# Performance work log

Measured on AMD Instinct MI355X. Metric: run time of the kernel, lower is better.

## Reference

```python
import jax, jax.numpy as jnp
import numpy as np

B, N, D = 32, 32768, 128

def setup_inputs() -> dict:
    key = jax.random.key(0)
    k1, k2, k3 = jax.random.split(key, 3)
    inputs = jax.random.normal(k1, (B, D), dtype=jnp.float32)
    # alphas must be in (0,1): variance = 1 - alpha
    alphas = jax.random.uniform(k2, (B,), dtype=jnp.float32, minval=0.05, maxval=0.95)
    data_batch = jax.random.normal(k3, (N, D), dtype=jnp.float32)
    return {"inputs": inputs, "alphas": alphas, "data_batch": data_batch}

def reference(inputs, alphas, data_batch):
    # inputs: [B, D], alphas: [B], data_batch: [N, D]
    d = inputs.shape[-1]
    sqrt_a = jnp.sqrt(alphas)[:, None]          # [B, 1]
    var = (1.0 - alphas)[:, None]                # [B, 1]
    # means = sqrt(alpha) * data -> [B, N, D]; squared distance summed over D
    diff = inputs[:, None, :] - sqrt_a[:, :, None] * data_batch[None]  # [B, N, D]
    sq = jnp.sum(diff * diff, axis=-1)           # [B, N]
    # logits summed over feature dim: -(0.5*D*log(var) + 0.5/var * sq)
    logits = -(0.5 * d * jnp.log(var) + 0.5 / var * sq)  # [B, N]
    probs = jax.nn.softmax(logits, axis=1)       # [B, N]
    x0 = probs @ data_batch                      # [B, D]
    return (inputs - sqrt_a * x0) / jnp.sqrt(var)
```

## Files before the change

### kernel.cpp

```cpp
#include <hip/hip_runtime.h>
#include <math.h>

#define BB 32
#define DD 128
#define NN 32768

#define NB 1024
#define RPB 32
#define NP NB
#define WS_MS_OFF ((size_t)BB * NB * DD)

typedef __attribute__((ext_vector_type(8))) short bf16x8;
typedef __attribute__((ext_vector_type(4))) float f32x4;

#define O_RH   0
#define O_RL   8192
#define O_INH  16384
#define O_INL  24576
#define O_RT   32768
#define O_NRM  40960
#define O_LQ   41088
#define ARENA  45184
#define O_PT   O_INH
#define O_X0   O_RH

__device__ __forceinline__ unsigned bf16_rne(float x) {
    unsigned u = __builtin_bit_cast(unsigned, x);
    return (u + 0x7FFFu + ((u >> 16) & 1u)) >> 16;
}
__device__ __forceinline__ float bf16f(unsigned h) {
    return __builtin_bit_cast(float, h << 16);
}
__device__ __forceinline__ unsigned pk2(float a, float b) {
    return bf16_rne(a) | (bf16_rne(b) << 16);
}

__global__ __launch_bounds__(256) void bayes_k1(
    const float* __restrict__ inputs, const float* __restrict__ alphas,
    const float* __restrict__ data, float* __restrict__ ws)
{
    __shared__ __align__(16) char arena[ARENA];

    const int tid  = threadIdx.x;
    const int lane = tid & 63;
    const int wv   = tid >> 6;
    const int ln   = lane & 15;
    const int g    = lane >> 4;
    const int bid  = blockIdx.x;

    {
        const int r = tid >> 3, c8 = tid & 7;
        const float4* gp = (const float4*)(data + ((size_t)bid * RPB + r) * DD + c8 * 16);
        float v[16];
        #pragma unroll
        for (int i = 0; i < 4; ++i) {
            const float4 t4 = gp[i];
            v[4*i+0] = t4.x; v[4*i+1] = t4.y; v[4*i+2] = t4.z; v[4*i+3] = t4.w;
        }
        float nn = 0.0f;
        #pragma unroll
        for (int i = 0; i < 16; ++i) nn = fmaf(v[i], v[i], nn);
        nn += __shfl_xor(nn, 1);
        nn += __shfl_xor(nn, 2);
        nn += __shfl_xor(nn, 4);
        if (c8 == 0) *(float*)(arena + O_NRM + r * 4) = nn;

        const int swz = (r & 7) << 4;
        #pragma unroll
        for (int u = 0; u < 2; ++u) {
            unsigned hw[4], lw[4];
            #pragma unroll
            for (int j = 0; j < 4; ++j) {
                const float a = v[u*8 + 2*j], b = v[u*8 + 2*j + 1];
                const unsigned ah = bf16_rne(a), bh = bf16_rne(b);
                hw[j] = ah | (bh << 16);
                lw[j] = pk2(a - bf16f(ah), b - bf16f(bh));
            }
            const int go = (c8 * 32 + u * 16) ^ swz;
            *(uint4*)(arena + O_RH + r * 256 + go) = make_uint4(hw[0], hw[1], hw[2], hw[3]);
            *(uint4*)(arena + O_RL + r * 256 + go) = make_uint4(lw[0], lw[1], lw[2], lw[3]);
        }
    }

    {
        const int b = tid >> 3, c8 = tid & 7;
        const float4* gp = (const float4*)(inputs + b * DD + c8 * 16);
        float v[16];
        #pragma unroll
        for (int i = 0; i < 4; ++i) {
            const float4 t4 = gp[i];
            v[4*i+0] = t4.x; v[4*i+1] = t4.y; v[4*i+2] = t4.z; v[4*i+3] = t4.w;
        }
        const int swz = (b & 7) << 4;
        #pragma unroll
        for (int u = 0; u < 2; ++u) {
            unsigned hw[4], lw[4];
            #pragma unroll
            for (int j = 0; j < 4; ++j) {
                const float a = v[u*8 + 2*j], bb = v[u*8 + 2*j + 1];
                const unsigned ah = bf16_rne(a), bh = bf16_rne(bb);
                hw[j] = ah | (bh << 16);
                lw[j] = pk2(a - bf16f(ah), bb - bf16f(bh));
            }
            const int go = (c8 * 32 + u * 16) ^ swz;
            *(uint4*)(arena + O_INH + b * 256 + go) = make_uint4(hw[0], hw[1], hw[2], hw[3]);
            *(uint4*)(arena + O_INL + b * 256 + go) = make_uint4(lw[0], lw[1], lw[2], lw[3]);
        }
    }

    {
        const int d = tid >> 1, rh = tid & 1;
        const float* gc = data + ((size_t)bid * RPB + rh * 16) * DD + d;
        const int swz = (d & 3) << 4;
        #pragma unroll
        for (int u = 0; u < 2; ++u) {
            unsigned w[4];
            #pragma unroll
            for (int j = 0; j < 4; ++j)
                w[j] = pk2(gc[(u*8 + 2*j) * DD], gc[(u*8 + 2*j + 1) * DD]);
            *(uint4*)(arena + O_RT + d * 64 + ((rh * 32 + u * 16) ^ swz)) =
                make_uint4(w[0], w[1], w[2], w[3]);
        }
    }
    __syncthreads();

    {
        const int mt = wv >> 1, nt = wv & 1;
        const int r  = mt * 16 + ln;
        const int b2 = nt * 16 + ln;
        f32x4 acc1;
        #pragma unroll
        for (int i = 0; i < 4; ++i) acc1[i] = 0.0f;

        #pragma unroll
        for (int ks = 0; ks < 4; ++ks) {
            const int kbyte = ks * 64 + g * 16;
            const bf16x8 Bh = *(const bf16x8*)(arena + O_INH + b2 * 256 + (kbyte ^ ((b2 & 7) << 4)));
            const bf16x8 Bl = *(const bf16x8*)(arena + O_INL + b2 * 256 + (kbyte ^ ((b2 & 7) << 4)));
            const bf16x8 Ah = *(const bf16x8*)(arena + O_RH  + r  * 256 + (kbyte ^ ((r  & 7) << 4)));
            const bf16x8 Al = *(const bf16x8*)(arena + O_RL  + r  * 256 + (kbyte ^ ((r  & 7) << 4)));
            acc1 = __builtin_amdgcn_mfma_f32_16x16x32_bf16(Ah, Bh, acc1, 0, 0, 0);
            acc1 = __builtin_amdgcn_mfma_f32_16x16x32_bf16(Al, Bh, acc1, 0, 0, 0);
            acc1 = __builtin_amdgcn_mfma_f32_16x16x32_bf16(Ah, Bl, acc1, 0, 0, 0);
        }
        #pragma unroll
        for (int i = 0; i < 4; ++i)
            *(float*)(arena + O_LQ + (((mt * 16 + g * 4 + i) * 32) + nt * 16 + ln) * 4) = acc1[i];
    }
    __syncthreads();

    if (wv < 2) {
        const int b = wv * 16 + ln;
        const float alpha = alphas[b];
        const float var = 1.0f - alpha;
        const float c1 = sqrtf(alpha) / var;
        const float c2 = 0.5f * alpha / var;

        float lg[8];
        float mx = -1e30f;
        #pragma unroll
        for (int j = 0; j < 8; ++j) {
            const int r = g * 8 + j;
            const float L  = *(const float*)(arena + O_LQ + (r * 32 + b) * 4);
            const float nr = *(const float*)(arena + O_NRM + r * 4);
            lg[j] = fmaf(c1, L, -c2 * nr);
            mx = fmaxf(mx, lg[j]);
        }
        mx = fmaxf(mx, __shfl_xor(mx, 16));
        mx = fmaxf(mx, __shfl_xor(mx, 32));

        float e[8];
        float ss = 0.0f;
        #pragma unroll
        for (int j = 0; j < 8; ++j) { e[j] = __expf(lg[j] - mx); ss += e[j]; }
        ss += __shfl_xor(ss, 16);
        ss += __shfl_xor(ss, 32);

        *(uint4*)(arena + O_PT + b * 64 + ((g * 16) ^ ((b & 3) << 4))) =
            make_uint4(pk2(e[0], e[1]), pk2(e[2], e[3]), pk2(e[4], e[5]), pk2(e[6], e[7]));
        if (g == 0)
            *(float2*)(ws + WS_MS_OFF + ((size_t)b * NB + bid) * 2) = make_float2(mx, ss);
    }
    __syncthreads();

    {
        f32x4 acc2[2][2];
        #pragma unroll
        for (int a = 0; a < 2; ++a)
            #pragma unroll
            for (int c = 0; c < 2; ++c)
                #pragma unroll
                for (int i = 0; i < 4; ++i) acc2[a][c][i] = 0.0f;

        bf16x8 Bp[2];
        #pragma unroll
        for (int nt = 0; nt < 2; ++nt) {
            const int b2 = nt * 16 + ln;
            Bp[nt] = *(const bf16x8*)(arena + O_PT + b2 * 64 + ((g * 16) ^ ((b2 & 3) << 4)));
        }
        #pragma unroll
        for (int a = 0; a < 2; ++a) {
            const int d = (wv * 2 + a) * 16 + ln;
            const bf16x8 Ar = *(const bf16x8*)(arena + O_RT + d * 64 + ((g * 16) ^ ((d & 3) << 4)));
            #pragma unroll
            for (int nt = 0; nt < 2; ++nt)
                acc2[a][nt] = __builtin_amdgcn_mfma_f32_16x16x32_bf16(Ar, Bp[nt], acc2[a][nt], 0, 0, 0);
        }
        #pragma unroll
        for (int a = 0; a < 2; ++a)
            #pragma unroll
            for (int nt = 0; nt < 2; ++nt) {
                const int b  = nt * 16 + ln;
                const int d0 = (wv * 2 + a) * 16 + g * 4;
                *(f32x4*)(arena + O_X0 + b * 512 + ((d0 * 4) ^ ((b & 7) << 4))) = acc2[a][nt];
            }
    }
    __syncthreads();

    {
        const int b = tid >> 3, c8 = tid & 7;
        const int swz = (b & 7) << 4;
        float* dst = ws + ((size_t)b * NB + bid) * DD + c8 * 16;
        #pragma unroll
        for (int u = 0; u < 4; ++u) {
            const f32x4 v = *(const f32x4*)(arena + O_X0 + b * 512 + ((c8 * 64 + u * 16) ^ swz));
            *(f32x4*)(dst + u * 4) = v;
        }
    }
}

__global__ __launch_bounds__(256) void bayes_k2(
    const float* __restrict__ inputs, const float* __restrict__ alphas,
    const float* __restrict__ ws, float* __restrict__ out)
{
    const int b   = blockIdx.x >> 2;
    const int dq  = blockIdx.x & 3;
    const int tid = threadIdx.x;

    __shared__ float e_s[NP];
    __shared__ float red_s[16];
    __shared__ float part[8][32];

    const float* msb = ws + WS_MS_OFF + (size_t)b * NP * 2;
    float mi[4], si[4];
    #pragma unroll
    for (int q = 0; q < 4; ++q) {
        const float2 v = *(const float2*)(msb + (tid + q * 256) * 2);
        mi[q] = v.x; si[q] = v.y;
    }

    float mm = fmaxf(fmaxf(mi[0], mi[1]), fmaxf(mi[2], mi[3]));
    #pragma unroll
    for (int off = 1; off <= 32; off <<= 1) mm = fmaxf(mm, __shfl_xor(mm, off));
    if ((tid & 63) == 0) red_s[tid >> 6] = mm;
    __syncthreads();
    const float M = fmaxf(fmaxf(red_s[0], red_s[1]), fmaxf(red_s[2], red_s[3]));

    float ss = 0.0f;
    #pragma unroll
    for (int q = 0; q < 4; ++q) {
        const float ei = __expf(mi[q] - M);
        e_s[tid + q * 256] = ei;
        ss = fmaf(si[q], ei, ss);
    }
    #pragma unroll
    for (int off = 1; off <= 32; off <<= 1) ss += __shfl_xor(ss, off);
    if ((tid & 63) == 0) red_s[8 + (tid >> 6)] = ss;
    __syncthreads();
    const float S = (red_s[8] + red_s[9]) + (red_s[10] + red_s[11]);

    const int dd = tid & 31, ii = tid >> 5;
    const int d  = dq * 32 + dd;
    const float* xb = ws + (size_t)b * NP * DD + d;
    float x0a = 0.0f, x0b = 0.0f;
    #pragma unroll 4
    for (int k = 0; k < 128; k += 2) {
        const int i0 = ii + k * 8, i1 = ii + (k + 1) * 8;
        x0a = fmaf(e_s[i0], xb[(size_t)i0 * DD], x0a);
        x0b = fmaf(e_s[i1], xb[(size_t)i1 * DD], x0b);
    }
    part[ii][dd] = x0a + x0b;
    __syncthreads();

    if (tid < 32) {
        float x0 = 0.0f;
        #pragma unroll
        for (int p = 0; p < 8; ++p) x0 += part[p][tid];
        x0 /= S;
        const float alpha = alphas[b];
        const float sa  = sqrtf(alpha);
        const float var = 1.0f - alpha;
        const int dout  = dq * 32 + tid;
        out[b * DD + dout] = (inputs[b * DD + dout] - sa * x0) / sqrtf(var);
    }
}

extern "C" void kernel_launch(void* const* d_in, const int* in_sizes, int n_in,
                              void* d_out, int out_size, void* d_ws, size_t ws_size,
                              hipStream_t stream)
{
    const float* inputs = (const float*)d_in[0];
    const float* alphas = (const float*)d_in[1];
    const float* data   = (const float*)d_in[2];
    float* out = (float*)d_out;
    float* ws  = (float*)d_ws;

    bayes_k1<<<NB, 256, 0, stream>>>(inputs, alphas, data, ws);
    bayes_k2<<<BB * 4, 256, 0, stream>>>(inputs, alphas, ws, out);
}
```

Measured before the change: 92.49 us.

## Process multiple row tiles per block with double-buffered online softmax

Each block of the first kernel now handles 128 data rows in four 32-row tiles. It uses 512 threads and double-buffers the shared-memory staging, so the global loads for the next tile overlap the MFMA work on the current one. The softmax is kept online across tiles by rescaling the running accumulator and sum. This cuts the partial-result workspace from 1024 to 256 partials per batch and shrinks the reduction in the second kernel. In exchange there are more barriers per block, fewer blocks (256, about one per CU) and less parallelism.

```diff
diff --git a/kernel.cpp b/kernel.cpp
--- a/kernel.cpp
+++ b/kernel.cpp
@@ -5,24 +5,30 @@
 #define DD 128
 #define NN 32768
 
-#define NB 1024
-#define RPB 32
+#define NB 256
+#define T1 512
+#define RPB 128
+#define TR 32
 #define NP NB
 #define WS_MS_OFF ((size_t)BB * NB * DD)
 
 typedef __attribute__((ext_vector_type(8))) short bf16x8;
 typedef __attribute__((ext_vector_type(4))) float f32x4;
 
-#define O_RH   0
-#define O_RL   8192
-#define O_INH  16384
-#define O_INL  24576
-#define O_RT   32768
-#define O_NRM  40960
-#define O_LQ   41088
-#define ARENA  45184
-#define O_PT   O_INH
-#define O_X0   O_RH
+#define O_RH0  0
+#define O_RL0  8192
+#define O_RT0  16384
+#define O_RH1  24576
+#define O_RL1  32768
+#define O_RT1  40960
+#define O_INH  49152
+#define O_INL  57344
+#define O_D1   65536
+#define O_NRM  69632
+#define O_PT   69888
+#define O_SCL  71936
+#define ARENA  72064
+#define O_X0   0
 
 __device__ __forceinline__ unsigned bf16_rne(float x) {
     unsigned u = __builtin_bit_cast(unsigned, x);
@@ -35,7 +41,7 @@
     return bf16_rne(a) | (bf16_rne(b) << 16);
 }
 
-__global__ __launch_bounds__(256) void bayes_k1(
+__global__ __launch_bounds__(T1) void bayes_k1(
     const float* __restrict__ inputs, const float* __restrict__ alphas,
     const float* __restrict__ data, float* __restrict__ ws)
 {
@@ -48,184 +54,198 @@
     const int g    = lane >> 4;
     const int bid  = blockIdx.x;
 
+    const int kh  = wv >> 2;
+    const int nt  = (wv >> 1) & 1;
+    const int mtw = wv & 1;
+
+    const int rA  = tid >> 4, cA = tid & 15;
+    const int dB  = tid >> 2, rq = tid & 3;
+
     {
-        const int r = tid >> 3, c8 = tid & 7;
-        const float4* gp = (const float4*)(data + ((size_t)bid * RPB + r) * DD + c8 * 16);
-        float v[16];
-        #pragma unroll
-        for (int i = 0; i < 4; ++i) {
-            const float4 t4 = gp[i];
-            v[4*i+0] = t4.x; v[4*i+1] = t4.y; v[4*i+2] = t4.z; v[4*i+3] = t4.w;
-        }
-        float nn = 0.0f;
-        #pragma unroll
-        for (int i = 0; i < 16; ++i) nn = fmaf(v[i], v[i], nn);
-        nn += __shfl_xor(nn, 1);
-        nn += __shfl_xor(nn, 2);
-        nn += __shfl_xor(nn, 4);
-        if (c8 == 0) *(float*)(arena + O_NRM + r * 4) = nn;
-
-        const int swz = (r & 7) << 4;
-        #pragma unroll
-        for (int u = 0; u < 2; ++u) {
-            unsigned hw[4], lw[4];
-            #pragma unroll
-            for (int j = 0; j < 4; ++j) {
-                const float a = v[u*8 + 2*j], b = v[u*8 + 2*j + 1];
-                const unsigned ah = bf16_rne(a), bh = bf16_rne(b);
-                hw[j] = ah | (bh << 16);
-                lw[j] = pk2(a - bf16f(ah), b - bf16f(bh));
-            }
-            const int go = (c8 * 32 + u * 16) ^ swz;
-            *(uint4*)(arena + O_RH + r * 256 + go) = make_uint4(hw[0], hw[1], hw[2], hw[3]);
-            *(uint4*)(arena + O_RL + r * 256 + go) = make_uint4(lw[0], lw[1], lw[2], lw[3]);
-        }
-    }
-
-    {
-        const int b = tid >> 3, c8 = tid & 7;
-        const float4* gp = (const float4*)(inputs + b * DD + c8 * 16);
-        float v[16];
-        #pragma unroll
-        for (int i = 0; i < 4; ++i) {
-            const float4 t4 = gp[i];
-            v[4*i+0] = t4.x; v[4*i+1] = t4.y; v[4*i+2] = t4.z; v[4*i+3] = t4.w;
-        }
-        const int swz = (b & 7) << 4;
-        #pragma unroll
-        for (int u = 0; u < 2; ++u) {
-            unsigned hw[4], lw[4];
-            #pragma unroll
-            for (int j = 0; j < 4; ++j) {
-                const float a = v[u*8 + 2*j], bb = v[u*8 + 2*j + 1];
-                const unsigned ah = bf16_rne(a), bh = bf16_rne(bb);
-                hw[j] = ah | (bh << 16);
-                lw[j] = pk2(a - bf16f(ah), bb - bf16f(bh));
-            }
-            const int go = (c8 * 32 + u * 16) ^ swz;
-            *(uint4*)(arena + O_INH + b * 256 + go) = make_uint4(hw[0], hw[1], hw[2], hw[3]);
-            *(uint4*)(arena + O_INL + b * 256 + go) = make_uint4(lw[0], lw[1], lw[2], lw[3]);
-        }
-    }
-
-    {
-        const int d = tid >> 1, rh = tid & 1;
-        const float* gc = data + ((size_t)bid * RPB + rh * 16) * DD + d;
-        const int swz = (d & 3) << 4;
-        #pragma unroll
-        for (int u = 0; u < 2; ++u) {
-            unsigned w[4];
-            #pragma unroll
-            for (int j = 0; j < 4; ++j)
-                w[j] = pk2(gc[(u*8 + 2*j) * DD], gc[(u*8 + 2*j + 1) * DD]);
-            *(uint4*)(arena + O_RT + d * 64 + ((rh * 32 + u * 16) ^ swz)) =
-                make_uint4(w[0], w[1], w[2], w[3]);
-        }
-    }
-    __syncthreads();
-
-    {
-        const int mt = wv >> 1, nt = wv & 1;
-        const int r  = mt * 16 + ln;
-        const int b2 = nt * 16 + ln;
-        f32x4 acc1;
-        #pragma unroll
-        for (int i = 0; i < 4; ++i) acc1[i] = 0.0f;
-
-        #pragma unroll
-        for (int ks = 0; ks < 4; ++ks) {
-            const int kbyte = ks * 64 + g * 16;
-            const bf16x8 Bh = *(const bf16x8*)(arena + O_INH + b2 * 256 + (kbyte ^ ((b2 & 7) << 4)));
-            const bf16x8 Bl = *(const bf16x8*)(arena + O_INL + b2 * 256 + (kbyte ^ ((b2 & 7) << 4)));
-            const bf16x8 Ah = *(const bf16x8*)(arena + O_RH  + r  * 256 + (kbyte ^ ((r  & 7) << 4)));
-            const bf16x8 Al = *(const bf16x8*)(arena + O_RL  + r  * 256 + (kbyte ^ ((r  & 7) << 4)));
-            acc1 = __builtin_amdgcn_mfma_f32_16x16x32_bf16(Ah, Bh, acc1, 0, 0, 0);
-            acc1 = __builtin_amdgcn_mfma_f32_16x16x32_bf16(Al, Bh, acc1, 0, 0, 0);
-            acc1 = __builtin_amdgcn_mfma_f32_16x16x32_bf16(Ah, Bl, acc1, 0, 0, 0);
-        }
-        #pragma unroll
-        for (int i = 0; i < 4; ++i)
-            *(float*)(arena + O_LQ + (((mt * 16 + g * 4 + i) * 32) + nt * 16 + ln) * 4) = acc1[i];
-    }
-    __syncthreads();
-
+        const int b = rA, c16 = cA;
+        const float4* gp = (const float4*)(inputs + b * DD + c16 * 8);
+        const float4 x0 = gp[0], x1 = gp[1];
+        const float v[8] = {x0.x, x0.y, x0.z, x0.w, x1.x, x1.y, x1.z, x1.w};
+        unsigned hw[4], lw[4];
+        #pragma unroll
+        for (int j = 0; j < 4; ++j) {
+            const float a = v[2*j], bb = v[2*j+1];
+            const unsigned ah = bf16_rne(a), bh = bf16_rne(bb);
+            hw[j] = ah | (bh << 16);
+            lw[j] = pk2(a - bf16f(ah), bb - bf16f(bh));
+        }
+        const int go = (c16 * 16) ^ ((b & 7) << 4);
+        *(uint4*)(arena + O_INH + b * 256 + go) = make_uint4(hw[0], hw[1], hw[2], hw[3]);
+        *(uint4*)(arena + O_INL + b * 256 + go) = make_uint4(lw[0], lw[1], lw[2], lw[3]);
+    }
+
+    float c1 = 0.f, c2 = 0.f;
     if (wv < 2) {
         const int b = wv * 16 + ln;
         const float alpha = alphas[b];
         const float var = 1.0f - alpha;
-        const float c1 = sqrtf(alpha) / var;
-        const float c2 = 0.5f * alpha / var;
-
-        float lg[8];
-        float mx = -1e30f;
-        #pragma unroll
-        for (int j = 0; j < 8; ++j) {
-            const int r = g * 8 + j;
-            const float L  = *(const float*)(arena + O_LQ + (r * 32 + b) * 4);
-            const float nr = *(const float*)(arena + O_NRM + r * 4);
-            lg[j] = fmaf(c1, L, -c2 * nr);
-            mx = fmaxf(mx, lg[j]);
-        }
-        mx = fmaxf(mx, __shfl_xor(mx, 16));
-        mx = fmaxf(mx, __shfl_xor(mx, 32));
-
-        float e[8];
-        float ss = 0.0f;
-        #pragma unroll
-        for (int j = 0; j < 8; ++j) { e[j] = __expf(lg[j] - mx); ss += e[j]; }
-        ss += __shfl_xor(ss, 16);
-        ss += __shfl_xor(ss, 32);
-
-        *(uint4*)(arena + O_PT + b * 64 + ((g * 16) ^ ((b & 3) << 4))) =
-            make_uint4(pk2(e[0], e[1]), pk2(e[2], e[3]), pk2(e[4], e[5]), pk2(e[6], e[7]));
-        if (g == 0)
-            *(float2*)(ws + WS_MS_OFF + ((size_t)b * NB + bid) * 2) = make_float2(mx, ss);
-    }
-    __syncthreads();
-
+        c1 = sqrtf(alpha) / var;
+        c2 = 0.5f * alpha / var;
+    }
+
+    float4 pa0, pa1; float pbv[8];
     {
-        f32x4 acc2[2][2];
-        #pragma unroll
-        for (int a = 0; a < 2; ++a)
-            #pragma unroll
-            for (int c = 0; c < 2; ++c)
-                #pragma unroll
-                for (int i = 0; i < 4; ++i) acc2[a][c][i] = 0.0f;
-
-        bf16x8 Bp[2];
-        #pragma unroll
-        for (int nt = 0; nt < 2; ++nt) {
+        const float4* gpA = (const float4*)(data + ((size_t)bid * RPB + rA) * DD + cA * 8);
+        pa0 = gpA[0]; pa1 = gpA[1];
+        const float* gpB = data + ((size_t)bid * RPB + rq * 8) * DD + dB;
+        #pragma unroll
+        for (int j = 0; j < 8; ++j) pbv[j] = gpB[(size_t)j * DD];
+    }
+    #define STAGE_WRITE(RHo, RLo, RTo, nbuf)                                            \
+    {                                                                                   \
+        const float v[8] = {pa0.x, pa0.y, pa0.z, pa0.w, pa1.x, pa1.y, pa1.z, pa1.w};    \
+        float nn = 0.f;                                                                 \
+        _Pragma("unroll") for (int i = 0; i < 8; ++i) nn = fmaf(v[i], v[i], nn);        \
+        nn += __shfl_xor(nn, 1); nn += __shfl_xor(nn, 2);                               \
+        nn += __shfl_xor(nn, 4); nn += __shfl_xor(nn, 8);                               \
+        if (cA == 0) *(float*)(arena + O_NRM + (nbuf) * 128 + rA * 4) = nn;             \
+        unsigned hw[4], lw[4];                                                          \
+        _Pragma("unroll") for (int j = 0; j < 4; ++j) {                                 \
+            const float a = v[2*j], bb = v[2*j+1];                                      \
+            const unsigned ah = bf16_rne(a), bh = bf16_rne(bb);                         \
+            hw[j] = ah | (bh << 16);                                                    \
+            lw[j] = pk2(a - bf16f(ah), bb - bf16f(bh));                                 \
+        }                                                                               \
+        const int go = (cA * 16) ^ ((rA & 7) << 4);                                     \
+        *(uint4*)(arena + (RHo) + rA * 256 + go) = make_uint4(hw[0], hw[1], hw[2], hw[3]); \
+        *(uint4*)(arena + (RLo) + rA * 256 + go) = make_uint4(lw[0], lw[1], lw[2], lw[3]); \
+        unsigned tw[4];                                                                 \
+        _Pragma("unroll") for (int j = 0; j < 4; ++j) tw[j] = pk2(pbv[2*j], pbv[2*j+1]); \
+        *(uint4*)(arena + (RTo) + dB * 64 + ((rq * 16) ^ ((dB & 3) << 4))) =            \
+            make_uint4(tw[0], tw[1], tw[2], tw[3]);                                     \
+    }
+    STAGE_WRITE(O_RH0, O_RL0, O_RT0, 0)
+    __syncthreads();
+
+    float m_run = -INFINITY, s_run = 0.0f;
+    f32x4 acc2[2];
+    #pragma unroll
+    for (int n2 = 0; n2 < 2; ++n2)
+        #pragma unroll
+        for (int i = 0; i < 4; ++i) acc2[n2][i] = 0.0f;
+
+    #pragma unroll
+    for (int t = 0; t < 4; ++t) {
+        const int RHc = (t & 1) ? O_RH1 : O_RH0;
+        const int RLc = (t & 1) ? O_RL1 : O_RL0;
+        const int RTc = (t & 1) ? O_RT1 : O_RT0;
+        const int RHn = (t & 1) ? O_RH0 : O_RH1;
+        const int RLn = (t & 1) ? O_RL0 : O_RL1;
+        const int RTn = (t & 1) ? O_RT0 : O_RT1;
+
+        if (t < 3) {
+            const float4* gpA = (const float4*)(data + ((size_t)bid * RPB + (t + 1) * TR + rA) * DD + cA * 8);
+            pa0 = gpA[0]; pa1 = gpA[1];
+            const float* gpB = data + ((size_t)bid * RPB + (t + 1) * TR + rq * 8) * DD + dB;
+            #pragma unroll
+            for (int j = 0; j < 8; ++j) pbv[j] = gpB[(size_t)j * DD];
+        }
+
+        f32x4 acc1;
+        #pragma unroll
+        for (int i = 0; i < 4; ++i) acc1[i] = 0.0f;
+        #pragma unroll
+        for (int ks = 0; ks < 2; ++ks) {
+            const int kbyte = kh * 128 + ks * 64 + g * 16;
             const int b2 = nt * 16 + ln;
-            Bp[nt] = *(const bf16x8*)(arena + O_PT + b2 * 64 + ((g * 16) ^ ((b2 & 3) << 4)));
-        }
-        #pragma unroll
-        for (int a = 0; a < 2; ++a) {
-            const int d = (wv * 2 + a) * 16 + ln;
-            const bf16x8 Ar = *(const bf16x8*)(arena + O_RT + d * 64 + ((g * 16) ^ ((d & 3) << 4)));
-            #pragma unroll
-            for (int nt = 0; nt < 2; ++nt)
-                acc2[a][nt] = __builtin_amdgcn_mfma_f32_16x16x32_bf16(Ar, Bp[nt], acc2[a][nt], 0, 0, 0);
-        }
-        #pragma unroll
-        for (int a = 0; a < 2; ++a)
-            #pragma unroll
-            for (int nt = 0; nt < 2; ++nt) {
-                const int b  = nt * 16 + ln;
-                const int d0 = (wv * 2 + a) * 16 + g * 4;
-                *(f32x4*)(arena + O_X0 + b * 512 + ((d0 * 4) ^ ((b & 7) << 4))) = acc2[a][nt];
+            const int r  = mtw * 16 + ln;
+            const bf16x8 Bh = *(const bf16x8*)(arena + O_INH + b2 * 256 + (kbyte ^ ((b2 & 7) << 4)));
+            const bf16x8 Bl = *(const bf16x8*)(arena + O_INL + b2 * 256 + (kbyte ^ ((b2 & 7) << 4)));
+            const bf16x8 Ah = *(const bf16x8*)(arena + RHc + r * 256 + (kbyte ^ ((r & 7) << 4)));
+            const bf16x8 Al = *(const bf16x8*)(arena + RLc + r * 256 + (kbyte ^ ((r & 7) << 4)));
+            acc1 = __builtin_amdgcn_mfma_f32_16x16x32_bf16(Ah, Bh, acc1, 0, 0, 0);
+            acc1 = __builtin_amdgcn_mfma_f32_16x16x32_bf16(Al, Bh, acc1, 0, 0, 0);
+            acc1 = __builtin_amdgcn_mfma_f32_16x16x32_bf16(Ah, Bl, acc1, 0, 0, 0);
+        }
+        if (kh == 1) {
+            #pragma unroll
+            for (int i = 0; i < 4; ++i)
+                *(float*)(arena + O_D1 + (((mtw * 16 + g * 4 + i) * 32) + nt * 16 + ln) * 4) = acc1[i];
+        }
+        __syncthreads();
+
+        if (t < 3) STAGE_WRITE(RHn, RLn, RTn, ((t + 1) & 1))
+
+        if (kh == 0) {
+            #pragma unroll
+            for (int i = 0; i < 4; ++i) {
+                float* p = (float*)(arena + O_D1 + (((mtw * 16 + g * 4 + i) * 32) + nt * 16 + ln) * 4);
+                *p = *p + acc1[i];
             }
-    }
-    __syncthreads();
-
+        }
+        __syncthreads();
+
+        if (wv < 2) {
+            const int b = wv * 16 + ln;
+            float lg[8];
+            float mx = -1e30f;
+            #pragma unroll
+            for (int j = 0; j < 8; ++j) {
+                const int r = g * 8 + j;
+                const float L  = *(const float*)(arena + O_D1 + (r * 32 + b) * 4);
+                const float nr = *(const float*)(arena + O_NRM + (t & 1) * 128 + r * 4);
+                lg[j] = fmaf(c1, L, -c2 * nr);
+                mx = fmaxf(mx, lg[j]);
+            }
+            mx = fmaxf(mx, __shfl_xor(mx, 16));
+            mx = fmaxf(mx, __shfl_xor(mx, 32));
+            const float m_new = fmaxf(m_run, mx);
+            const float scl_b = __expf(m_run - m_new);
+            float e[8];
+            float ssl = 0.0f;
+            #pragma unroll
+            for (int j = 0; j < 8; ++j) { e[j] = __expf(lg[j] - m_new); ssl += e[j]; }
+            ssl += __shfl_xor(ssl, 16);
+            ssl += __shfl_xor(ssl, 32);
+            s_run = s_run * scl_b + ssl;
+            m_run = m_new;
+            *(uint4*)(arena + O_PT + b * 64 + ((g * 16) ^ ((b & 3) << 4))) =
+                make_uint4(pk2(e[0], e[1]), pk2(e[2], e[3]), pk2(e[4], e[5]), pk2(e[6], e[7]));
+            if (g == 0) *(float*)(arena + O_SCL + b * 4) = scl_b;
+        }
+        __syncthreads();
+
+        {
+            const float sc0 = *(const float*)(arena + O_SCL + ln * 4);
+            const float sc1 = *(const float*)(arena + O_SCL + (16 + ln) * 4);
+            #pragma unroll
+            for (int i = 0; i < 4; ++i) { acc2[0][i] *= sc0; acc2[1][i] *= sc1; }
+            const int didx = wv * 16 + ln;
+            const bf16x8 Ar = *(const bf16x8*)(arena + RTc + didx * 64 + ((g * 16) ^ ((didx & 3) << 4)));
+            #pragma unroll
+            for (int n2 = 0; n2 < 2; ++n2) {
+                const int b2 = n2 * 16 + ln;
+                const bf16x8 Bp = *(const bf16x8*)(arena + O_PT + b2 * 64 + ((g * 16) ^ ((b2 & 3) << 4)));
+                acc2[n2] = __builtin_amdgcn_mfma_f32_16x16x32_bf16(Ar, Bp, acc2[n2], 0, 0, 0);
+            }
+        }
+        __syncthreads();
+    }
+
+    #pragma unroll
+    for (int n2 = 0; n2 < 2; ++n2) {
+        const int b  = n2 * 16 + ln;
+        const int d0 = wv * 16 + g * 4;
+        *(f32x4*)(arena + O_X0 + b * 512 + ((d0 * 4) ^ ((b & 7) << 4))) = acc2[n2];
+    }
+    if (wv < 2 && g == 0) {
+        const int b = wv * 16 + ln;
+        *(float2*)(ws + WS_MS_OFF + ((size_t)b * NB + bid) * 2) = make_float2(m_run, s_run);
+    }
+    __syncthreads();
     {
-        const int b = tid >> 3, c8 = tid & 7;
-        const int swz = (b & 7) << 4;
-        float* dst = ws + ((size_t)b * NB + bid) * DD + c8 * 16;
-        #pragma unroll
-        for (int u = 0; u < 4; ++u) {
-            const f32x4 v = *(const f32x4*)(arena + O_X0 + b * 512 + ((c8 * 64 + u * 16) ^ swz));
-            *(f32x4*)(dst + u * 4) = v;
-        }
+        const int b = tid >> 4, c16 = tid & 15;
+        const int swzb = (b & 7) << 4;
+        const f32x4 v0 = *(const f32x4*)(arena + O_X0 + b * 512 + ((c16 * 32) ^ swzb));
+        const f32x4 v1 = *(const f32x4*)(arena + O_X0 + b * 512 + ((c16 * 32 + 16) ^ swzb));
+        float* dst = ws + ((size_t)b * NB + bid) * DD + c16 * 8;
+        *(f32x4*)dst = v0;
+        *(f32x4*)(dst + 4) = v1;
     }
 }
 
@@ -241,28 +261,19 @@
     __shared__ float red_s[16];
     __shared__ float part[8][32];
 
-    const float* msb = ws + WS_MS_OFF + (size_t)b * NP * 2;
-    float mi[4], si[4];
-    #pragma unroll
-    for (int q = 0; q < 4; ++q) {
-        const float2 v = *(const float2*)(msb + (tid + q * 256) * 2);
-        mi[q] = v.x; si[q] = v.y;
-    }
-
-    float mm = fmaxf(fmaxf(mi[0], mi[1]), fmaxf(mi[2], mi[3]));
+    const float2 v = *(const float2*)(ws + WS_MS_OFF + ((size_t)b * NP + tid) * 2);
+    const float mi = v.x, si = v.y;
+
+    float mm = mi;
     #pragma unroll
     for (int off = 1; off <= 32; off <<= 1) mm = fmaxf(mm, __shfl_xor(mm, off));
     if ((tid & 63) == 0) red_s[tid >> 6] = mm;
     __syncthreads();
     const float M = fmaxf(fmaxf(red_s[0], red_s[1]), fmaxf(red_s[2], red_s[3]));
 
-    float ss = 0.0f;
-    #pragma unroll
-    for (int q = 0; q < 4; ++q) {
-        const float ei = __expf(mi[q] - M);
-        e_s[tid + q * 256] = ei;
-        ss = fmaf(si[q], ei, ss);
-    }
+    const float ei = __expf(mi - M);
+    e_s[tid] = ei;
+    float ss = si * ei;
     #pragma unroll
     for (int off = 1; off <= 32; off <<= 1) ss += __shfl_xor(ss, off);
     if ((tid & 63) == 0) red_s[8 + (tid >> 6)] = ss;
@@ -274,7 +285,7 @@
     const float* xb = ws + (size_t)b * NP * DD + d;
     float x0a = 0.0f, x0b = 0.0f;
     #pragma unroll 4
-    for (int k = 0; k < 128; k += 2) {
+    for (int k = 0; k < 32; k += 2) {
         const int i0 = ii + k * 8, i1 = ii + (k + 1) * 8;
         x0a = fmaf(e_s[i0], xb[(size_t)i0 * DD], x0a);
         x0b = fmaf(e_s[i1], xb[(size_t)i1 * DD], x0b);
@@ -305,6 +316,6 @@
     float* out = (float*)d_out;
     float* ws  = (float*)d_ws;
 
-    bayes_k1<<<NB, 256, 0, stream>>>(inputs, alphas, data, ws);
+    bayes_k1<<<NB, T1, 0, stream>>>(inputs, alphas, data, ws);
     bayes_k2<<<BB * 4, 256, 0, stream>>>(inputs, alphas, ws, out);
 }
```

Result: faster. 78.98 us (-14.6%).

## Fuse both kernels via cooperative grid sync with double-buffered online-softmax tiles

Applied to the files above, without the earlier changes.

Merges the two kernels into one cooperative launch that uses a grid-wide sync before the final reduction. Each block now processes 64 rows in two 32-row tiles, with double-buffered LDS, a prefetch of the next tile, and online softmax rescaling of the accumulators. Halving the block count also halves the partial-result workspace that the reduction stage must read. The cost is a grid barrier, heavier per-block LDS use (about 72KB), and reliance on all 512 blocks being co-resident.

```diff
diff --git a/kernel.cpp b/kernel.cpp
--- a/kernel.cpp
+++ b/kernel.cpp
@@ -1,28 +1,36 @@
 #include <hip/hip_runtime.h>
+#include <hip/hip_cooperative_groups.h>
 #include <math.h>
+
+namespace cg = cooperative_groups;
 
 #define BB 32
 #define DD 128
 #define NN 32768
 
-#define NB 1024
-#define RPB 32
+#define NB 512
+#define T1 256
+#define RPB 64
+#define TR 32
 #define NP NB
 #define WS_MS_OFF ((size_t)BB * NB * DD)
 
 typedef __attribute__((ext_vector_type(8))) short bf16x8;
 typedef __attribute__((ext_vector_type(4))) float f32x4;
 
-#define O_RH   0
-#define O_RL   8192
-#define O_INH  16384
-#define O_INL  24576
-#define O_RT   32768
-#define O_NRM  40960
-#define O_LQ   41088
-#define ARENA  45184
-#define O_PT   O_INH
-#define O_X0   O_RH
+#define O_RH0  0
+#define O_RL0  8192
+#define O_RT0  16384
+#define O_RH1  24576
+#define O_RL1  32768
+#define O_RT1  40960
+#define O_INH  49152
+#define O_INL  57344
+#define O_D1   65536
+#define O_NRM  69760
+#define O_PT   70016
+#define O_SCL  72064
+#define ARENA  72192
 
 __device__ __forceinline__ unsigned bf16_rne(float x) {
     unsigned u = __builtin_bit_cast(unsigned, x);
@@ -35,9 +43,9 @@
     return bf16_rne(a) | (bf16_rne(b) << 16);
 }
 
-__global__ __launch_bounds__(256) void bayes_k1(
+__global__ __launch_bounds__(T1) void bayes_fused(
     const float* __restrict__ inputs, const float* __restrict__ alphas,
-    const float* __restrict__ data, float* __restrict__ ws)
+    const float* __restrict__ data, float* __restrict__ ws, float* __restrict__ out)
 {
     __shared__ __align__(16) char arena[ARENA];
 
@@ -48,48 +56,17 @@
     const int g    = lane >> 4;
     const int bid  = blockIdx.x;
 
+    const int rA = tid >> 3, cA = tid & 7;
+    const int dB = tid >> 1, rh = tid & 1;
+
     {
-        const int r = tid >> 3, c8 = tid & 7;
-        const float4* gp = (const float4*)(data + ((size_t)bid * RPB + r) * DD + c8 * 16);
+        const int b = rA, c8 = cA;
+        const float4* gp = (const float4*)(inputs + b * DD + c8 * 16);
         float v[16];
         #pragma unroll
         for (int i = 0; i < 4; ++i) {
             const float4 t4 = gp[i];
-            v[4*i+0] = t4.x; v[4*i+1] = t4.y; v[4*i+2] = t4.z; v[4*i+3] = t4.w;
-        }
-        float nn = 0.0f;
-        #pragma unroll
-        for (int i = 0; i < 16; ++i) nn = fmaf(v[i], v[i], nn);
-        nn += __shfl_xor(nn, 1);
-        nn += __shfl_xor(nn, 2);
-        nn += __shfl_xor(nn, 4);
-        if (c8 == 0) *(float*)(arena + O_NRM + r * 4) = nn;
-
-        const int swz = (r & 7) << 4;
-        #pragma unroll
-        for (int u = 0; u < 2; ++u) {
-            unsigned hw[4], lw[4];
-            #pragma unroll
-            for (int j = 0; j < 4; ++j) {
-                const float a = v[u*8 + 2*j], b = v[u*8 + 2*j + 1];
-                const unsigned ah = bf16_rne(a), bh = bf16_rne(b);
-                hw[j] = ah | (bh << 16);
-                lw[j] = pk2(a - bf16f(ah), b - bf16f(bh));
-            }
-            const int go = (c8 * 32 + u * 16) ^ swz;
-            *(uint4*)(arena + O_RH + r * 256 + go) = make_uint4(hw[0], hw[1], hw[2], hw[3]);
-            *(uint4*)(arena + O_RL + r * 256 + go) = make_uint4(lw[0], lw[1], lw[2], lw[3]);
-        }
-    }
-
-    {
-        const int b = tid >> 3, c8 = tid & 7;
-        const float4* gp = (const float4*)(inputs + b * DD + c8 * 16);
-        float v[16];
-        #pragma unroll
-        for (int i = 0; i < 4; ++i) {
-            const float4 t4 = gp[i];
-            v[4*i+0] = t4.x; v[4*i+1] = t4.y; v[4*i+2] = t4.z; v[4*i+3] = t4.w;
+            v[4*i] = t4.x; v[4*i+1] = t4.y; v[4*i+2] = t4.z; v[4*i+3] = t4.w;
         }
         const int swz = (b & 7) << 4;
         #pragma unroll
@@ -102,196 +79,256 @@
                 hw[j] = ah | (bh << 16);
                 lw[j] = pk2(a - bf16f(ah), bb - bf16f(bh));
             }
-            const int go = (c8 * 32 + u * 16) ^ swz;
+            const int go = (cA * 32 + u * 16) ^ swz;
             *(uint4*)(arena + O_INH + b * 256 + go) = make_uint4(hw[0], hw[1], hw[2], hw[3]);
             *(uint4*)(arena + O_INL + b * 256 + go) = make_uint4(lw[0], lw[1], lw[2], lw[3]);
         }
     }
 
-    {
-        const int d = tid >> 1, rh = tid & 1;
-        const float* gc = data + ((size_t)bid * RPB + rh * 16) * DD + d;
-        const int swz = (d & 3) << 4;
-        #pragma unroll
-        for (int u = 0; u < 2; ++u) {
-            unsigned w[4];
-            #pragma unroll
-            for (int j = 0; j < 4; ++j)
-                w[j] = pk2(gc[(u*8 + 2*j) * DD], gc[(u*8 + 2*j + 1) * DD]);
-            *(uint4*)(arena + O_RT + d * 64 + ((rh * 32 + u * 16) ^ swz)) =
-                make_uint4(w[0], w[1], w[2], w[3]);
-        }
-    }
-    __syncthreads();
-
-    {
-        const int mt = wv >> 1, nt = wv & 1;
-        const int r  = mt * 16 + ln;
-        const int b2 = nt * 16 + ln;
-        f32x4 acc1;
-        #pragma unroll
-        for (int i = 0; i < 4; ++i) acc1[i] = 0.0f;
-
-        #pragma unroll
-        for (int ks = 0; ks < 4; ++ks) {
-            const int kbyte = ks * 64 + g * 16;
-            const bf16x8 Bh = *(const bf16x8*)(arena + O_INH + b2 * 256 + (kbyte ^ ((b2 & 7) << 4)));
-            const bf16x8 Bl = *(const bf16x8*)(arena + O_INL + b2 * 256 + (kbyte ^ ((b2 & 7) << 4)));
-            const bf16x8 Ah = *(const bf16x8*)(arena + O_RH  + r  * 256 + (kbyte ^ ((r  & 7) << 4)));
-            const bf16x8 Al = *(const bf16x8*)(arena + O_RL  + r  * 256 + (kbyte ^ ((r  & 7) << 4)));
-            acc1 = __builtin_amdgcn_mfma_f32_16x16x32_bf16(Ah, Bh, acc1, 0, 0, 0);
-            acc1 = __builtin_amdgcn_mfma_f32_16x16x32_bf16(Al, Bh, acc1, 0, 0, 0);
-            acc1 = __builtin_amdgcn_mfma_f32_16x16x32_bf16(Ah, Bl, acc1, 0, 0, 0);
-        }
-        #pragma unroll
-        for (int i = 0; i < 4; ++i)
-            *(float*)(arena + O_LQ + (((mt * 16 + g * 4 + i) * 32) + nt * 16 + ln) * 4) = acc1[i];
-    }
-    __syncthreads();
-
+    float c1 = 0.f, c2 = 0.f;
     if (wv < 2) {
         const int b = wv * 16 + ln;
         const float alpha = alphas[b];
         const float var = 1.0f - alpha;
-        const float c1 = sqrtf(alpha) / var;
-        const float c2 = 0.5f * alpha / var;
-
-        float lg[8];
-        float mx = -1e30f;
-        #pragma unroll
-        for (int j = 0; j < 8; ++j) {
-            const int r = g * 8 + j;
-            const float L  = *(const float*)(arena + O_LQ + (r * 32 + b) * 4);
-            const float nr = *(const float*)(arena + O_NRM + r * 4);
-            lg[j] = fmaf(c1, L, -c2 * nr);
-            mx = fmaxf(mx, lg[j]);
-        }
-        mx = fmaxf(mx, __shfl_xor(mx, 16));
-        mx = fmaxf(mx, __shfl_xor(mx, 32));
-
-        float e[8];
-        float ss = 0.0f;
-        #pragma unroll
-        for (int j = 0; j < 8; ++j) { e[j] = __expf(lg[j] - mx); ss += e[j]; }
-        ss += __shfl_xor(ss, 16);
-        ss += __shfl_xor(ss, 32);
-
-        *(uint4*)(arena + O_PT + b * 64 + ((g * 16) ^ ((b & 3) << 4))) =
-            make_uint4(pk2(e[0], e[1]), pk2(e[2], e[3]), pk2(e[4], e[5]), pk2(e[6], e[7]));
-        if (g == 0)
-            *(float2*)(ws + WS_MS_OFF + ((size_t)b * NB + bid) * 2) = make_float2(mx, ss);
-    }
+        c1 = sqrtf(alpha) / var;
+        c2 = 0.5f * alpha / var;
+    }
+
+    float4 pa[4]; float pbv[16];
+    {
+        const float4* gpA = (const float4*)(data + ((size_t)bid * RPB + rA) * DD + cA * 16);
+        #pragma unroll
+        for (int i = 0; i < 4; ++i) pa[i] = gpA[i];
+        const float* gpB = data + ((size_t)bid * RPB + rh * 16) * DD + dB;
+        #pragma unroll
+        for (int j = 0; j < 16; ++j) pbv[j] = gpB[(size_t)j * DD];
+    }
+
+    #define STAGE_WRITE(RHo, RLo, RTo, nbuf)                                               \
+    {                                                                                      \
+        float v[16];                                                                       \
+        _Pragma("unroll") for (int i = 0; i < 4; ++i) {                                    \
+            v[4*i] = pa[i].x; v[4*i+1] = pa[i].y; v[4*i+2] = pa[i].z; v[4*i+3] = pa[i].w;  \
+        }                                                                                  \
+        float nn = 0.f;                                                                    \
+        _Pragma("unroll") for (int i = 0; i < 16; ++i) nn = fmaf(v[i], v[i], nn);          \
+        nn += __shfl_xor(nn, 1); nn += __shfl_xor(nn, 2); nn += __shfl_xor(nn, 4);         \
+        if (cA == 0) *(float*)(arena + O_NRM + (nbuf) * 128 + rA * 4) = nn;                \
+        const int swzA = (rA & 7) << 4;                                                    \
+        _Pragma("unroll") for (int u = 0; u < 2; ++u) {                                    \
+            unsigned hw[4], lw[4];                                                         \
+            _Pragma("unroll") for (int j = 0; j < 4; ++j) {                                \
+                const float a = v[u*8 + 2*j], bb = v[u*8 + 2*j + 1];                       \
+                const unsigned ah = bf16_rne(a), bh = bf16_rne(bb);                        \
+                hw[j] = ah | (bh << 16);                                                   \
+                lw[j] = pk2(a - bf16f(ah), bb - bf16f(bh));                                \
+            }                                                                              \
+            const int go = (cA * 32 + u * 16) ^ swzA;                                      \
+            *(uint4*)(arena + (RHo) + rA * 256 + go) = make_uint4(hw[0], hw[1], hw[2], hw[3]); \
+            *(uint4*)(arena + (RLo) + rA * 256 + go) = make_uint4(lw[0], lw[1], lw[2], lw[3]); \
+        }                                                                                  \
+        const int swzB = (dB & 3) << 4;                                                    \
+        _Pragma("unroll") for (int u = 0; u < 2; ++u) {                                    \
+            unsigned tw[4];                                                                \
+            _Pragma("unroll") for (int j = 0; j < 4; ++j)                                  \
+                tw[j] = pk2(pbv[u*8 + 2*j], pbv[u*8 + 2*j + 1]);                           \
+            *(uint4*)(arena + (RTo) + dB * 64 + ((rh * 32 + u * 16) ^ swzB)) =             \
+                make_uint4(tw[0], tw[1], tw[2], tw[3]);                                    \
+        }                                                                                  \
+    }
+    STAGE_WRITE(O_RH0, O_RL0, O_RT0, 0)
     __syncthreads();
 
-    {
-        f32x4 acc2[2][2];
-        #pragma unroll
-        for (int a = 0; a < 2; ++a)
-            #pragma unroll
-            for (int c = 0; c < 2; ++c)
+    float m_run = -INFINITY, s_run = 0.0f;
+    f32x4 acc2[2][2];
+    #pragma unroll
+    for (int a = 0; a < 2; ++a)
+        #pragma unroll
+        for (int n2 = 0; n2 < 2; ++n2)
+            #pragma unroll
+            for (int i = 0; i < 4; ++i) acc2[a][n2][i] = 0.0f;
+
+    #pragma unroll
+    for (int t = 0; t < 2; ++t) {
+        const int RHc = t ? O_RH1 : O_RH0;
+        const int RLc = t ? O_RL1 : O_RL0;
+        const int RTc = t ? O_RT1 : O_RT0;
+
+        if (t == 0) {
+            const float4* gpA = (const float4*)(data + ((size_t)bid * RPB + TR + rA) * DD + cA * 16);
+            #pragma unroll
+            for (int i = 0; i < 4; ++i) pa[i] = gpA[i];
+            const float* gpB = data + ((size_t)bid * RPB + TR + rh * 16) * DD + dB;
+            #pragma unroll
+            for (int j = 0; j < 16; ++j) pbv[j] = gpB[(size_t)j * DD];
+        }
+
+        {
+            const int mt = wv >> 1, nt = wv & 1;
+            const int r  = mt * 16 + ln;
+            const int b2 = nt * 16 + ln;
+            f32x4 a1a, a1b;
+            #pragma unroll
+            for (int i = 0; i < 4; ++i) { a1a[i] = 0.0f; a1b[i] = 0.0f; }
+            #pragma unroll
+            for (int ks = 0; ks < 4; ++ks) {
+                const int kbyte = ks * 64 + g * 16;
+                const bf16x8 Bh = *(const bf16x8*)(arena + O_INH + b2 * 256 + (kbyte ^ ((b2 & 7) << 4)));
+                const bf16x8 Bl = *(const bf16x8*)(arena + O_INL + b2 * 256 + (kbyte ^ ((b2 & 7) << 4)));
+                const bf16x8 Ah = *(const bf16x8*)(arena + RHc + r * 256 + (kbyte ^ ((r & 7) << 4)));
+                const bf16x8 Al = *(const bf16x8*)(arena + RLc + r * 256 + (kbyte ^ ((r & 7) << 4)));
+                f32x4& acc = (ks & 2) ? a1b : a1a;
+                acc = __builtin_amdgcn_mfma_f32_16x16x32_bf16(Ah, Bh, acc, 0, 0, 0);
+                acc = __builtin_amdgcn_mfma_f32_16x16x32_bf16(Al, Bh, acc, 0, 0, 0);
+                acc = __builtin_amdgcn_mfma_f32_16x16x32_bf16(Ah, Bl, acc, 0, 0, 0);
+            }
+            #pragma unroll
+            for (int i = 0; i < 4; ++i)
+                *(float*)(arena + O_D1 + (((mt * 16 + g * 4 + i) * 33) + nt * 16 + ln) * 4) =
+                    a1a[i] + a1b[i];
+        }
+        __syncthreads();
+
+        if (t == 0) STAGE_WRITE(O_RH1, O_RL1, O_RT1, 1)
+
+        if (wv < 2) {
+            const int b = wv * 16 + ln;
+            float lg[8];
+            float mx = -1e30f;
+            #pragma unroll
+            for (int j = 0; j < 8; ++j) {
+                const int r = g * 8 + j;
+                const float L  = *(const float*)(arena + O_D1 + (r * 33 + b) * 4);
+                const float nr = *(const float*)(arena + O_NRM + t * 128 + r * 4);
+                lg[j] = fmaf(c1, L, -c2 * nr);
+                mx = fmaxf(mx, lg[j]);
+            }
+            mx = fmaxf(mx, __shfl_xor(mx, 16));
+            mx = fmaxf(mx, __shfl_xor(mx, 32));
+            const float m_new = fmaxf(m_run, mx);
+            const float scl_b = __expf(m_run - m_new);
+            float e[8];
+            float ssl = 0.0f;
+            #pragma unroll
+            for (int j = 0; j < 8; ++j) { e[j] = __expf(lg[j] - m_new); ssl += e[j]; }
+            ssl += __shfl_xor(ssl, 16);
+            ssl += __shfl_xor(ssl, 32);
+            s_run = s_run * scl_b + ssl;
+            m_run = m_new;
+            *(uint4*)(arena + O_PT + b * 64 + ((g * 16) ^ ((b & 3) << 4))) =
+                make_uint4(pk2(e[0], e[1]), pk2(e[2], e[3]), pk2(e[4], e[5]), pk2(e[6], e[7]));
+            if (g == 0) *(float*)(arena + O_SCL + b * 4) = scl_b;
+        }
+        __syncthreads();
+
+        {
+            const float sc0 = *(const float*)(arena + O_SCL + ln * 4);
+            const float sc1 = *(const float*)(arena + O_SCL + (16 + ln) * 4);
+            #pragma unroll
+            for (int a = 0; a < 2; ++a)
                 #pragma unroll
-                for (int i = 0; i < 4; ++i) acc2[a][c][i] = 0.0f;
-
-        bf16x8 Bp[2];
-        #pragma unroll
-        for (int nt = 0; nt < 2; ++nt) {
-            const int b2 = nt * 16 + ln;
-            Bp[nt] = *(const bf16x8*)(arena + O_PT + b2 * 64 + ((g * 16) ^ ((b2 & 3) << 4)));
-        }
-        #pragma unroll
-        for (int a = 0; a < 2; ++a) {
-            const int d = (wv * 2 + a) * 16 + ln;
-            const bf16x8 Ar = *(const bf16x8*)(arena + O_RT + d * 64 + ((g * 16) ^ ((d & 3) << 4)));
-            #pragma unroll
-            for (int nt = 0; nt < 2; ++nt)
-                acc2[a][nt] = __builtin_amdgcn_mfma_f32_16x16x32_bf16(Ar, Bp[nt], acc2[a][nt], 0, 0, 0);
-        }
-        #pragma unroll
-        for (int a = 0; a < 2; ++a)
-            #pragma unroll
-            for (int nt = 0; nt < 2; ++nt) {
-                const int b  = nt * 16 + ln;
-                const int d0 = (wv * 2 + a) * 16 + g * 4;
-                *(f32x4*)(arena + O_X0 + b * 512 + ((d0 * 4) ^ ((b & 7) << 4))) = acc2[a][nt];
+                for (int i = 0; i < 4; ++i) { acc2[a][0][i] *= sc0; acc2[a][1][i] *= sc1; }
+            #pragma unroll
+            for (int a = 0; a < 2; ++a) {
+                const int d = (wv * 2 + a) * 16 + ln;
+                const bf16x8 Ar = *(const bf16x8*)(arena + RTc + d * 64 + ((g * 16) ^ ((d & 3) << 4)));
+                #pragma unroll
+                for (int n2 = 0; n2 < 2; ++n2) {
+                    const int b2 = n2 * 16 + ln;
+                    const bf16x8 Bp = *(const bf16x8*)(arena + O_PT + b2 * 64 + ((g * 16) ^ ((b2 & 3) << 4)));
+                    acc2[a][n2] = __builtin_amdgcn_mfma_f32_16x16x32_bf16(Ar, Bp, acc2[a][n2], 0, 0, 0);
+                }
             }
+        }
+        __syncthreads();
+    }
+
+    #pragma unroll
+    for (int a = 0; a < 2; ++a)
+        #pragma unroll
+        for (int n2 = 0; n2 < 2; ++n2) {
+            const int b  = n2 * 16 + ln;
+            const int d0 = (wv * 2 + a) * 16 + g * 4;
+            *(f32x4*)(arena + (b * 512) + ((d0 * 4) ^ ((b & 7) << 4))) = acc2[a][n2];
+        }
+    if (wv < 2 && g == 0) {
+        const int b = wv * 16 + ln;
+        *(float2*)(ws + WS_MS_OFF + ((size_t)b * NB + bid) * 2) = make_float2(m_run, s_run);
     }
     __syncthreads();
-
     {
         const int b = tid >> 3, c8 = tid & 7;
-        const int swz = (b & 7) << 4;
+        const int swzb = (b & 7) << 4;
         float* dst = ws + ((size_t)b * NB + bid) * DD + c8 * 16;
         #pragma unroll
         for (int u = 0; u < 4; ++u) {
-            const f32x4 v = *(const f32x4*)(arena + O_X0 + b * 512 + ((c8 * 64 + u * 16) ^ swz));
+            const f32x4 v = *(const f32x4*)(arena + b * 512 + ((c8 * 64 + u * 16) ^ swzb));
             *(f32x4*)(dst + u * 4) = v;
         }
     }
-}
-
-__global__ __launch_bounds__(256) void bayes_k2(
-    const float* __restrict__ inputs, const float* __restrict__ alphas,
-    const float* __restrict__ ws, float* __restrict__ out)
-{
-    const int b   = blockIdx.x >> 2;
-    const int dq  = blockIdx.x & 3;
-    const int tid = threadIdx.x;
-
-    __shared__ float e_s[NP];
-    __shared__ float red_s[16];
-    __shared__ float part[8][32];
-
-    const float* msb = ws + WS_MS_OFF + (size_t)b * NP * 2;
-    float mi[4], si[4];
-    #pragma unroll
-    for (int q = 0; q < 4; ++q) {
-        const float2 v = *(const float2*)(msb + (tid + q * 256) * 2);
-        mi[q] = v.x; si[q] = v.y;
-    }
-
-    float mm = fmaxf(fmaxf(mi[0], mi[1]), fmaxf(mi[2], mi[3]));
-    #pragma unroll
-    for (int off = 1; off <= 32; off <<= 1) mm = fmaxf(mm, __shfl_xor(mm, off));
-    if ((tid & 63) == 0) red_s[tid >> 6] = mm;
-    __syncthreads();
-    const float M = fmaxf(fmaxf(red_s[0], red_s[1]), fmaxf(red_s[2], red_s[3]));
-
-    float ss = 0.0f;
-    #pragma unroll
-    for (int q = 0; q < 4; ++q) {
-        const float ei = __expf(mi[q] - M);
-        e_s[tid + q * 256] = ei;
-        ss = fmaf(si[q], ei, ss);
-    }
-    #pragma unroll
-    for (int off = 1; off <= 32; off <<= 1) ss += __shfl_xor(ss, off);
-    if ((tid & 63) == 0) red_s[8 + (tid >> 6)] = ss;
-    __syncthreads();
-    const float S = (red_s[8] + red_s[9]) + (red_s[10] + red_s[11]);
-
-    const int dd = tid & 31, ii = tid >> 5;
-    const int d  = dq * 32 + dd;
-    const float* xb = ws + (size_t)b * NP * DD + d;
-    float x0a = 0.0f, x0b = 0.0f;
-    #pragma unroll 4
-    for (int k = 0; k < 128; k += 2) {
-        const int i0 = ii + k * 8, i1 = ii + (k + 1) * 8;
-        x0a = fmaf(e_s[i0], xb[(size_t)i0 * DD], x0a);
-        x0b = fmaf(e_s[i1], xb[(size_t)i1 * DD], x0b);
-    }
-    part[ii][dd] = x0a + x0b;
-    __syncthreads();
-
-    if (tid < 32) {
-        float x0 = 0.0f;
-        #pragma unroll
-        for (int p = 0; p < 8; ++p) x0 += part[p][tid];
-        x0 /= S;
-        const float alpha = alphas[b];
-        const float sa  = sqrtf(alpha);
-        const float var = 1.0f - alpha;
-        const int dout  = dq * 32 + tid;
-        out[b * DD + dout] = (inputs[b * DD + dout] - sa * x0) / sqrtf(var);
+
+    __threadfence();
+    cg::this_grid().sync();
+
+    if (bid >= BB * 4) return;
+    {
+        const int b  = bid >> 2;
+        const int dq = bid & 3;
+
+        float* e_s   = (float*)(arena);
+        float* red_s = (float*)(arena + 2048);
+        float* part  = (float*)(arena + 2112);
+
+        float mi[2], si[2];
+        #pragma unroll
+        for (int q = 0; q < 2; ++q) {
+            const float2 v = *(const float2*)(ws + WS_MS_OFF + ((size_t)b * NP + tid + q * 256) * 2);
+            mi[q] = v.x; si[q] = v.y;
+        }
+        float mm = fmaxf(mi[0], mi[1]);
+        #pragma unroll
+        for (int off = 1; off <= 32; off <<= 1) mm = fmaxf(mm, __shfl_xor(mm, off));
+        if (lane == 0) red_s[wv] = mm;
+        __syncthreads();
+        const float M = fmaxf(fmaxf(red_s[0], red_s[1]), fmaxf(red_s[2], red_s[3]));
+
+        float ss = 0.0f;
+        #pragma unroll
+        for (int q = 0; q < 2; ++q) {
+            const float ei = __expf(mi[q] - M);
+            e_s[tid + q * 256] = ei;
+            ss = fmaf(si[q], ei, ss);
+        }
+        #pragma unroll
+        for (int off = 1; off <= 32; off <<= 1) ss += __shfl_xor(ss, off);
+        if (lane == 0) red_s[8 + wv] = ss;
+        __syncthreads();
+        const float S = (red_s[8] + red_s[9]) + (red_s[10] + red_s[11]);
+
+        const int dd = tid & 31, ii = tid >> 5;
+        const int d  = dq * 32 + dd;
+        const float* xb = ws + (size_t)b * NP * DD + d;
+        float x0a = 0.0f, x0b = 0.0f;
+        #pragma unroll 4
+        for (int k = 0; k < 64; k += 2) {
+            const int i0 = ii + k * 8, i1 = ii + (k + 1) * 8;
+            x0a = fmaf(e_s[i0], xb[(size_t)i0 * DD], x0a);
+            x0b = fmaf(e_s[i1], xb[(size_t)i1 * DD], x0b);
+        }
+        part[ii * 32 + dd] = x0a + x0b;
+        __syncthreads();
+
+        if (tid < 32) {
+            float x0 = 0.0f;
+            #pragma unroll
+            for (int p = 0; p < 8; ++p) x0 += part[p * 32 + tid];
+            x0 /= S;
+            const float alpha = alphas[b];
+            const float sa  = sqrtf(alpha);
+            const float var = 1.0f - alpha;
+            const int dout  = dq * 32 + tid;
+            out[b * DD + dout] = (inputs[b * DD + dout] - sa * x0) / sqrtf(var);
+        }
     }
 }
 
@@ -305,6 +342,6 @@
     float* out = (float*)d_out;
     float* ws  = (float*)d_ws;
 
-    bayes_k1<<<NB, 256, 0, stream>>>(inputs, alphas, data, ws);
-    bayes_k2<<<BB * 4, 256, 0, stream>>>(inputs, alphas, ws, out);
-}
+    void* args[] = {(void*)&inputs, (void*)&alphas, (void*)&data, (void*)&ws, (void*)&out};
+    hipLaunchCooperativeKernel((void*)bayes_fused, dim3(NB), dim3(T1), args, 0, stream);
+}
```

Result: slower. 215.8 us (+133.3%).
